# Kernel tuning notes

Measured on AMD Instinct MI355X. Metric: run time of the kernel, lower is better.

## Reference

```python
import jax, jax.numpy as jnp
import numpy as np

D = 768


def _rope(x):
    # interleaved RoPE over the FULL hidden dim (applied before head split, as in source)
    S, d = x.shape[-2], x.shape[-1]
    pos = jnp.arange(S, dtype=x.dtype)[:, None]                      # [S,1]
    theta = jnp.power(jnp.asarray(10000.0, x.dtype),
                      -2.0 * jnp.arange(d // 2, dtype=x.dtype) / d)  # [d/2]
    ang = pos * theta                                                # [S,d/2]
    cos2 = jnp.repeat(jnp.cos(ang), 2, axis=-1)                      # [S,d]
    sin2 = jnp.repeat(jnp.sin(ang), 2, axis=-1)
    x2 = jnp.stack([-x[..., 1::2], x[..., ::2]], axis=-1).reshape(x.shape)
    return x * cos2 + x2 * sin2


def _attn(q_in, kv_in, wq, bq, wk, bk, wv, bv, n_heads):
    # shared core of SelfAttention (n_heads=1) and MultiheadAttention (n_heads=8)
    B, Sq, Dm = q_in.shape
    Sk = kv_in.shape[1]
    Q = _rope(q_in @ wq + bq)
    K = _rope(kv_in @ wk + bk)
    V = kv_in @ wv + bv
    hd = Dm // n_heads
    Q = Q.reshape(B, Sq, n_heads, hd).transpose(0, 2, 1, 3)
    K = K.reshape(B, Sk, n_heads, hd).transpose(0, 2, 1, 3)
    V = V.reshape(B, Sk, n_heads, hd).transpose(0, 2, 1, 3)
    scores = jnp.einsum('bhqd,bhkd->bhqk', Q, K) * 8.0  # source multiplies by 8, no 1/sqrt(d)
    p = jax.nn.softmax(scores, axis=-1)
    out = jnp.einsum('bhqk,bhkd->bhqd', p, V)
    return out.transpose(0, 2, 1, 3).reshape(B, Sq, Dm)


def _ffn(x, w1, b1, w2, b2):
    return jax.nn.silu(x @ w1 + b1) @ w2 + b2


def _gate(x):
    # F = F * softmax(F, -1) + F
    return x * jax.nn.softmax(x, axis=-1) + x


def setup_inputs() -> dict:
    key = jax.random.key(0)
    ks = jax.random.split(key, 32)
    B, S, L = 32, 512, 100
    s = 1.0 / np.sqrt(D)

    def lin(k):
        kw, kb = jax.random.split(k)
        return (jax.random.normal(kw, (D, D), jnp.float32) * s,
                jax.random.normal(kb, (D,), jnp.float32) * 0.01)

    inp = {}
    inp['text_embedding'] = jax.random.normal(ks[0], (B, S, D), jnp.float32)
    inp['visual_ids'] = jax.random.randint(ks[1], (B, S), 0, L)
    inp['acoustic_ids'] = jax.random.randint(ks[2], (B, S), 0, L)
    # embedding tables (label_size+1 rows, last row is padding_idx -> zeros)
    vt = jax.random.normal(ks[3], (L + 1, D), jnp.float32)
    at = jax.random.normal(ks[4], (L + 1, D), jnp.float32)
    inp['vis_table'] = vt.at[L].set(0.0)
    inp['ac_table'] = at.at[L].set(0.0)
    (inp['hv_wq'], inp['hv_bq']) = lin(ks[5])
    (inp['hv_wk'], inp['hv_bk']) = lin(ks[6])
    (inp['hv_wv'], inp['hv_bv']) = lin(ks[7])
    (inp['ha_wq'], inp['ha_bq']) = lin(ks[8])
    (inp['ha_wk'], inp['ha_bk']) = lin(ks[9])
    (inp['ha_wv'], inp['ha_bv']) = lin(ks[10])
    (inp['ht_wq'], inp['ht_bq']) = lin(ks[11])
    (inp['ht_wk'], inp['ht_bk']) = lin(ks[12])
    (inp['ht_wv'], inp['ht_bv']) = lin(ks[13])
    (inp['ht_fcw'], inp['ht_fcb']) = lin(ks[14])
    (inp['ffn_w1'], inp['ffn_b1']) = lin(ks[15])
    (inp['ffn_w2'], inp['ffn_b2']) = lin(ks[16])
    kw, kb = jax.random.split(ks[17])
    inp['cat_w'] = jax.random.normal(kw, (2 * D, D), jnp.float32) * (1.0 / np.sqrt(2 * D))
    inp['cat_b'] = jax.random.normal(kb, (D,), jnp.float32) * 0.01
    return inp


def reference(text_embedding, vis_table, ac_table,
              hv_wq, hv_bq, hv_wk, hv_bk, hv_wv, hv_bv,
              ha_wq, ha_bq, ha_wk, ha_bk, ha_wv, ha_bv,
              ht_wq, ht_bq, ht_wk, ht_bk, ht_wv, ht_bv, ht_fcw, ht_fcb,
              ffn_w1, ffn_b1, ffn_w2, ffn_b2, cat_w, cat_b,
              visual_ids, acoustic_ids):
    hv = lambda q, kv: _attn(q, kv, hv_wq, hv_bq, hv_wk, hv_bk, hv_wv, hv_bv, 1)
    ha = lambda q, kv: _attn(q, kv, ha_wq, ha_bq, ha_wk, ha_bk, ha_wv, ha_bv, 1)

    visual_ = vis_table[visual_ids]       # [B,S,D]
    acoustic_ = ac_table[acoustic_ids]

    visual_ = hv(text_embedding, visual_)
    acoustic_ = ha(text_embedding, acoustic_)

    F1 = jnp.concatenate([visual_, acoustic_], axis=-1) @ cat_w + cat_b
    F1 = _ffn(_gate(F1), ffn_w1, ffn_b1, ffn_w2, ffn_b2)

    v = hv(visual_, acoustic_)
    a = ha(acoustic_, visual_)
    F2 = jnp.concatenate([v, a], axis=-1) @ cat_w + cat_b
    F2 = _ffn(_gate(F2), ffn_w1, ffn_b1, ffn_w2, ffn_b2)

    F3 = _attn(F1, text_embedding, ht_wq, ht_bq, ht_wk, ht_bk, ht_wv, ht_bv, 8)
    F3 = F3 @ ht_fcw + ht_fcb
    F3 = _ffn(_gate(F3), ffn_w1, ffn_b1, ffn_w2, ffn_b2)

    es = text_embedding + F1 + F2 + F3
    return _gate(es)
```

## Files before the change

kernel.cpp:

```cpp
#include <hip/hip_runtime.h>
#include <stdint.h>
#include <math.h>


typedef unsigned short USH;
typedef __attribute__((ext_vector_type(8))) short short8;
typedef __attribute__((ext_vector_type(4))) float floatx4;

#define MFMA16(a, b, c) __builtin_amdgcn_mfma_f32_16x16x32_bf16((a), (b), (c), 0, 0, 0)

static constexpr int NB = 32;
static constexpr int SS = 512;
static constexpr int DD = 768;
static constexpr int MM = NB * SS;

__device__ __forceinline__ float bf2f(USH h) {
    return __uint_as_float(((unsigned)h) << 16);
}
__device__ __forceinline__ USH f2bf(float x) {
    unsigned u = __float_as_uint(x);
    return (USH)((u + 0x7fffu + ((u >> 16) & 1u)) >> 16);
}
__device__ __forceinline__ void split3(float x, USH &h, USH &m, USH &l) {
    h = f2bf(x);
    const float r1 = x - bf2f(h);
    m = f2bf(r1);
    const float r2 = r1 - bf2f(m);
    l = f2bf(r2);
}
__device__ __forceinline__ void split3x8(const float* v, short8 &H, short8 &M, short8 &L) {
#pragma unroll
    for (int j = 0; j < 8; ++j) {
        USH h, m, l;
        split3(v[j], h, m, l);
        H[j] = (short)h; M[j] = (short)m; L[j] = (short)l;
    }
}
__device__ __forceinline__ uint2 pk4(USH a, USH b, USH c, USH d) {
    uint2 r;
    r.x = (unsigned)a | ((unsigned)b << 16);
    r.y = (unsigned)c | ((unsigned)d << 16);
    return r;
}

struct TransArgs {
    const float* in[13];
    USH* o0[13]; USH* o1[13]; USH* o2[13];
    int R[13];
};

__global__ __launch_bounds__(256) void trans_k(TransArgs a) {
    const int mi = blockIdx.z;
    const float* __restrict__ in = a.in[mi];
    USH* __restrict__ o0 = a.o0[mi];
    USH* __restrict__ o1 = a.o1[mi];
    USH* __restrict__ o2 = a.o2[mi];
    const int R = a.R[mi];
    const int bx = blockIdx.x, by = blockIdx.y;
    if (bx * 32 >= R) return;
    __shared__ float t[32][33];
    const int tx = threadIdx.x & 31, ty = threadIdx.x >> 5;
#pragma unroll
    for (int i = 0; i < 4; ++i)
        t[ty + i * 8][tx] = in[(size_t)(bx * 32 + ty + i * 8) * 768 + by * 32 + tx];
    __syncthreads();
#pragma unroll
    for (int i = 0; i < 4; ++i) {
        USH h, m, l;
        split3(t[tx][ty + i * 8], h, m, l);
        const size_t o = (size_t)(by * 32 + ty + i * 8) * R + bx * 32 + tx;
        o0[o] = h; o1[o] = m; o2[o] = l;
    }
}

__global__ __launch_bounds__(256) void gather_k(const int* __restrict__ ids,
                                                const float* __restrict__ table,
                                                float* __restrict__ dst) {
    const int g  = blockIdx.x * 256 + threadIdx.x;
    const int m  = g / 192;
    const int c4 = (g - m * 192) * 4;
    const int id = ids[m];
    *(float4*)(dst + (size_t)m * DD + c4) =
        *(const float4*)(table + (size_t)id * DD + c4);
}

__global__ __launch_bounds__(256) void gemm_k(
    const float* __restrict__ A0, const float* __restrict__ A1,
    const USH* __restrict__ B0, const USH* __restrict__ B1, const USH* __restrict__ B2,
    int ldb, const float* __restrict__ bias,
    float* __restrict__ C, int K, int act, int tout, int Mc)
{
    __shared__ __align__(16) USH sA0[4096], sA1[4096], sA2[4096];
    __shared__ __align__(16) USH sB0[4096], sB1[4096], sB2[4096];

    const int tid  = threadIdx.x;
    const int lane = tid & 63;
    const int w    = tid >> 6;
    const int quad = lane >> 4, l15 = lane & 15;
    const int wm = (w >> 1) * 64, wn = (w & 1) * 64;
    const int gm0 = blockIdx.x * 128, gn0 = blockIdx.y * 128;

    const int i0 = tid * 2, i1 = tid * 2 + 1;
    const int r0 = i0 >> 2, c0 = (i0 & 3) << 3;
    const int r1 = i1 >> 2, c1 = (i1 & 3) << 3;

    const floatx4 zero = {0.f, 0.f, 0.f, 0.f};
    floatx4 acc[4][4];
#pragma unroll
    for (int i = 0; i < 4; ++i)
#pragma unroll
        for (int j = 0; j < 4; ++j) acc[i][j] = zero;

    for (int k0 = 0; k0 < K; k0 += 32) {
        const float* __restrict__ A = (k0 < 768) ? A0 : A1;
        const int kof = (k0 < 768) ? k0 : (k0 - 768);

        *(uint4*)&sB0[r0 * 32 + c0] = *(const uint4*)(B0 + (size_t)(gn0 + r0) * ldb + k0 + c0);
        *(uint4*)&sB0[r1 * 32 + c1] = *(const uint4*)(B0 + (size_t)(gn0 + r1) * ldb + k0 + c1);
        *(uint4*)&sB1[r0 * 32 + c0] = *(const uint4*)(B1 + (size_t)(gn0 + r0) * ldb + k0 + c0);
        *(uint4*)&sB1[r1 * 32 + c1] = *(const uint4*)(B1 + (size_t)(gn0 + r1) * ldb + k0 + c1);
        *(uint4*)&sB2[r0 * 32 + c0] = *(const uint4*)(B2 + (size_t)(gn0 + r0) * ldb + k0 + c0);
        *(uint4*)&sB2[r1 * 32 + c1] = *(const uint4*)(B2 + (size_t)(gn0 + r1) * ldb + k0 + c1);

#pragma unroll
        for (int u = 0; u < 4; ++u) {
            const int idx = tid + u * 256;
            const int r = idx >> 3, c = (idx & 7) * 4;
            const float4 v = *(const float4*)(A + (size_t)(gm0 + r) * 768 + kof + c);
            USH h[4], m[4], l[4];
            split3(v.x, h[0], m[0], l[0]);
            split3(v.y, h[1], m[1], l[1]);
            split3(v.z, h[2], m[2], l[2]);
            split3(v.w, h[3], m[3], l[3]);
            *(uint2*)&sA0[r * 32 + c] = pk4(h[0], h[1], h[2], h[3]);
            *(uint2*)&sA1[r * 32 + c] = pk4(m[0], m[1], m[2], m[3]);
            *(uint2*)&sA2[r * 32 + c] = pk4(l[0], l[1], l[2], l[3]);
        }
        __syncthreads();

        short8 a0[4], a1f[4], a2[4], b0[4], b1f[4], b2[4];
#pragma unroll
        for (int t = 0; t < 4; ++t) {
            const int ao = (wm + t * 16 + l15) * 32 + quad * 8;
            const int bo = (wn + t * 16 + l15) * 32 + quad * 8;
            a0[t]  = *(const short8*)&sA0[ao];
            a1f[t] = *(const short8*)&sA1[ao];
            a2[t]  = *(const short8*)&sA2[ao];
            b0[t]  = *(const short8*)&sB0[bo];
            b1f[t] = *(const short8*)&sB1[bo];
            b2[t]  = *(const short8*)&sB2[bo];
        }
#pragma unroll
        for (int i = 0; i < 4; ++i)
#pragma unroll
            for (int j = 0; j < 4; ++j) acc[i][j] = MFMA16(a0[i],  b0[j],  acc[i][j]);
#pragma unroll
        for (int i = 0; i < 4; ++i)
#pragma unroll
            for (int j = 0; j < 4; ++j) acc[i][j] = MFMA16(a0[i],  b1f[j], acc[i][j]);
#pragma unroll
        for (int i = 0; i < 4; ++i)
#pragma unroll
            for (int j = 0; j < 4; ++j) acc[i][j] = MFMA16(a1f[i], b0[j],  acc[i][j]);
#pragma unroll
        for (int i = 0; i < 4; ++i)
#pragma unroll
            for (int j = 0; j < 4; ++j) acc[i][j] = MFMA16(a0[i],  b2[j],  acc[i][j]);
#pragma unroll
        for (int i = 0; i < 4; ++i)
#pragma unroll
            for (int j = 0; j < 4; ++j) acc[i][j] = MFMA16(a2[i],  b0[j],  acc[i][j]);
#pragma unroll
        for (int i = 0; i < 4; ++i)
#pragma unroll
            for (int j = 0; j < 4; ++j) acc[i][j] = MFMA16(a1f[i], b1f[j], acc[i][j]);
        __syncthreads();
    }

#pragma unroll
    for (int j = 0; j < 4; ++j) {
        const int col = gn0 + wn + j * 16 + l15;
        const float bv = bias[col];
#pragma unroll
        for (int i = 0; i < 4; ++i) {
#pragma unroll
            for (int r = 0; r < 4; ++r) {
                const int row = gm0 + wm + i * 16 + quad * 4 + r;
                float x = acc[i][j][r] + bv;
                if (act == 1) {
                    const float s = 1.0f / (1.0f + expf(-x));
                    x = x * s;
                }
                const size_t o = tout ? ((size_t)col * Mc + row)
                                      : ((size_t)row * 768 + col);
                C[o] = x;
            }
        }
    }
}

__global__ __launch_bounds__(256) void rope_k(float* __restrict__ X) {
    const int p = blockIdx.x * 256 + threadIdx.x;
    const int m = p / 384;
    const int i = p - m * 384;
    const int s = m & (SS - 1);
    const float ef = (-2.0f * (float)i) / 768.0f;
    const float th = (float)pow(10000.0, (double)ef);
    const float ang = (float)s * th;
    float sn, cs;
    sincosf(ang, &sn, &cs);
    float2 x = *(float2*)(X + (size_t)m * DD + 2 * i);
    float2 y;
    y.x = x.x * cs - x.y * sn;
    y.y = x.y * cs + x.x * sn;
    *(float2*)(X + (size_t)m * DD + 2 * i) = y;
}

__global__ __launch_bounds__(256) void attn_k(
    const float* __restrict__ Q, const float* __restrict__ Kp,
    const float* __restrict__ Vt, float* __restrict__ O,
    int H, int hd, int Mc)
{
    __shared__ __align__(16) float S[16][520];
    __shared__ __align__(16) USH P2buf[16 * 520];
    __shared__ float red[16][16];
    __shared__ float stat[16];

    const int tid  = threadIdx.x;
    const int lane = tid & 63;
    const int w    = tid >> 6;
    const int quad = lane >> 4, l15 = lane & 15;
    const int b = blockIdx.y / H;
    const int h = blockIdx.y - b * H;
    const int q0 = blockIdx.x * 16;

    const floatx4 zero = {0.f, 0.f, 0.f, 0.f};

    floatx4 acc[8];
#pragma unroll
    for (int t = 0; t < 8; ++t) acc[t] = zero;

    const size_t qbase = ((size_t)(b * SS + q0 + l15)) * DD + h * hd;
    const int nks = hd >> 5;
    for (int ks = 0; ks < nks; ++ks) {
        const int co = ks * 32 + quad * 8;
        float qv[8];
        *(float4*)&qv[0] = *(const float4*)(Q + qbase + co);
        *(float4*)&qv[4] = *(const float4*)(Q + qbase + co + 4);
        short8 qh, qm, ql;
        split3x8(qv, qh, qm, ql);
#pragma unroll
        for (int t = 0; t < 8; ++t) {
            const size_t kb = ((size_t)(b * SS + w * 128 + t * 16 + l15)) * DD + h * hd + co;
            float kv[8];
            *(float4*)&kv[0] = *(const float4*)(Kp + kb);
            *(float4*)&kv[4] = *(const float4*)(Kp + kb + 4);
            short8 kh, km, kl;
            split3x8(kv, kh, km, kl);
            acc[t] = MFMA16(qh, kh, acc[t]);
            acc[t] = MFMA16(qh, km, acc[t]);
            acc[t] = MFMA16(qm, kh, acc[t]);
            acc[t] = MFMA16(qh, kl, acc[t]);
            acc[t] = MFMA16(ql, kh, acc[t]);
            acc[t] = MFMA16(qm, km, acc[t]);
        }
    }
#pragma unroll
    for (int t = 0; t < 8; ++t)
#pragma unroll
        for (int r = 0; r < 4; ++r)
            S[quad * 4 + r][w * 128 + t * 16 + l15] = acc[t][r] * 8.0f;
    __syncthreads();

    const int row = tid >> 4, c16 = tid & 15;
    const int cb = c16 * 32;
    float mx = -3.4e38f;
#pragma unroll 8
    for (int c = 0; c < 32; ++c) mx = fmaxf(mx, S[row][cb + c]);
    red[row][c16] = mx;
    __syncthreads();
    if (c16 == 0) {
        float m2 = red[row][0];
#pragma unroll
        for (int j = 1; j < 16; ++j) m2 = fmaxf(m2, red[row][j]);
        stat[row] = m2;
    }
    __syncthreads();
    mx = stat[row];
    float ev[32];
    float sum = 0.f;
#pragma unroll 8
    for (int c = 0; c < 32; ++c) {
        ev[c] = expf(S[row][cb + c] - mx);
        sum += ev[c];
    }
    red[row][c16] = sum;
    __syncthreads();
    if (c16 == 0) {
        float s2 = 0.f;
#pragma unroll
        for (int j = 0; j < 16; ++j) s2 += red[row][j];
        stat[row] = s2;
    }
    __syncthreads();
    const float den = stat[row];
    USH* const P0 = (USH*)&S[0][0];
    USH* const P1 = P0 + 16 * 520;
    USH* const P2 = P2buf;
#pragma unroll 8
    for (int c = 0; c < 32; ++c) {
        const float pr = ev[c] / den;
        USH hh, mm, ll;
        split3(pr, hh, mm, ll);
        P0[row * 520 + cb + c] = hh;
        P1[row * 520 + cb + c] = mm;
        P2[row * 520 + cb + c] = ll;
    }
    __syncthreads();

    const int nnt = hd >> 4;
    for (int nt = w; nt < nnt; nt += 4) {
        floatx4 o = zero;
        const int colg = h * hd + nt * 16 + l15;
        const size_t vb = (size_t)colg * Mc + b * SS;
        for (int ks = 0; ks < 16; ++ks) {
            const int ko = ks * 32 + quad * 8;
            const short8 ph = *(const short8*)&P0[l15 * 520 + ko];
            const short8 pm = *(const short8*)&P1[l15 * 520 + ko];
            const short8 pl = *(const short8*)&P2[l15 * 520 + ko];
            float vv[8];
            *(float4*)&vv[0] = *(const float4*)(Vt + vb + ko);
            *(float4*)&vv[4] = *(const float4*)(Vt + vb + ko + 4);
            short8 vh, vm, vl;
            split3x8(vv, vh, vm, vl);
            o = MFMA16(ph, vh, o);
            o = MFMA16(ph, vm, o);
            o = MFMA16(pm, vh, o);
            o = MFMA16(ph, vl, o);
            o = MFMA16(pl, vh, o);
            o = MFMA16(pm, vm, o);
        }
#pragma unroll
        for (int r = 0; r < 4; ++r) {
            const int orow = b * SS + q0 + quad * 4 + r;
            O[(size_t)orow * 768 + colg] = o[r];
        }
    }
}

__global__ __launch_bounds__(256) void gate_k(float* __restrict__ X) {
    __shared__ float red[256];
    const int r = blockIdx.x, tid = threadIdx.x;
    const size_t base = (size_t)r * DD;
    float x[3];
#pragma unroll
    for (int j = 0; j < 3; ++j) x[j] = X[base + tid + j * 256];
    float mx = fmaxf(x[0], fmaxf(x[1], x[2]));
    red[tid] = mx;
    __syncthreads();
    for (int s = 128; s > 0; s >>= 1) {
        if (tid < s) red[tid] = fmaxf(red[tid], red[tid + s]);
        __syncthreads();
    }
    mx = red[0];
    __syncthreads();
    float e[3];
    float sum = 0.f;
#pragma unroll
    for (int j = 0; j < 3; ++j) { e[j] = expf(x[j] - mx); sum += e[j]; }
    red[tid] = sum;
    __syncthreads();
    for (int s = 128; s > 0; s >>= 1) {
        if (tid < s) red[tid] += red[tid + s];
        __syncthreads();
    }
    const float den = red[0];
#pragma unroll
    for (int j = 0; j < 3; ++j)
        X[base + tid + j * 256] = x[j] * (e[j] / den) + x[j];
}

__global__ __launch_bounds__(256) void final_k(
    const float* __restrict__ text,
    const float* __restrict__ F1, const float* __restrict__ F2,
    const float* __restrict__ F3, float* __restrict__ out)
{
    __shared__ float red[256];
    const int r = blockIdx.x, tid = threadIdx.x;
    const size_t base = (size_t)r * DD;
    float x[3];
#pragma unroll
    for (int j = 0; j < 3; ++j) {
        const int c = tid + j * 256;
        x[j] = ((text[base + c] + F1[base + c]) + F2[base + c]) + F3[base + c];
    }
    float mx = fmaxf(x[0], fmaxf(x[1], x[2]));
    red[tid] = mx;
    __syncthreads();
    for (int s = 128; s > 0; s >>= 1) {
        if (tid < s) red[tid] = fmaxf(red[tid], red[tid + s]);
        __syncthreads();
    }
    mx = red[0];
    __syncthreads();
    float e[3];
    float sum = 0.f;
#pragma unroll
    for (int j = 0; j < 3; ++j) { e[j] = expf(x[j] - mx); sum += e[j]; }
    red[tid] = sum;
    __syncthreads();
    for (int s = 128; s > 0; s >>= 1) {
        if (tid < s) red[tid] += red[tid + s];
        __syncthreads();
    }
    const float den = red[0];
#pragma unroll
    for (int j = 0; j < 3; ++j) {
        const int c = tid + j * 256;
        out[base + c] = x[j] * (e[j] / den) + x[j];
    }
}

extern "C" void kernel_launch(void* const* d_in, const int* in_sizes, int n_in,
                              void* d_out, int out_size, void* d_ws, size_t ws_size,
                              hipStream_t stream)
{
    (void)in_sizes; (void)n_in; (void)out_size;

    const float* text    = (const float*)d_in[0];
    const int*   vis_ids = (const int*)d_in[1];
    const int*   ac_ids  = (const int*)d_in[2];
    const float* vis_tab = (const float*)d_in[3];
    const float* ac_tab  = (const float*)d_in[4];
    const float* hv_wq = (const float*)d_in[5],  *hv_bq = (const float*)d_in[6];
    const float* hv_wk = (const float*)d_in[7],  *hv_bk = (const float*)d_in[8];
    const float* hv_wv = (const float*)d_in[9],  *hv_bv = (const float*)d_in[10];
    const float* ha_wq = (const float*)d_in[11], *ha_bq = (const float*)d_in[12];
    const float* ha_wk = (const float*)d_in[13], *ha_bk = (const float*)d_in[14];
    const float* ha_wv = (const float*)d_in[15], *ha_bv = (const float*)d_in[16];
    const float* ht_wq = (const float*)d_in[17], *ht_bq = (const float*)d_in[18];
    const float* ht_wk = (const float*)d_in[19], *ht_bk = (const float*)d_in[20];
    const float* ht_wv = (const float*)d_in[21], *ht_bv = (const float*)d_in[22];
    const float* ht_fcw = (const float*)d_in[23], *ht_fcb = (const float*)d_in[24];
    const float* ffn_w1 = (const float*)d_in[25], *ffn_b1 = (const float*)d_in[26];
    const float* ffn_w2 = (const float*)d_in[27], *ffn_b2 = (const float*)d_in[28];
    const float* cat_w  = (const float*)d_in[29], *cat_b  = (const float*)d_in[30];

    const size_t SQ   = (size_t)768 * 768;
    const size_t WUSH = 3 * (12 * SQ + (size_t)768 * 1536);
    int Mc = 0;
    for (int cand = MM; cand >= 512; cand >>= 1) {
        const size_t need = WUSH * sizeof(USH) + (size_t)6 * cand * 768 * sizeof(float);
        if (need <= ws_size) { Mc = cand; break; }
    }
    if (Mc == 0) return;
    const int nchunk = MM / Mc;
    const int chB    = Mc / SS;

    USH* p = (USH*)d_ws;
    USH *wt0[13], *wt1[13], *wt2[13];
    for (int i = 0; i < 13; ++i) {
        const size_t sz = (i == 12) ? (size_t)768 * 1536 : SQ;
        wt0[i] = p; p += sz;
        wt1[i] = p; p += sz;
        wt2[i] = p; p += sz;
    }
    const size_t PSZ = (size_t)Mc * 768;
    float* fp = (float*)p;
    float *A_ = fp + 0 * PSZ, *B_ = fp + 1 * PSZ, *C_ = fp + 2 * PSZ;
    float *D_ = fp + 3 * PSZ, *E_ = fp + 4 * PSZ, *F_ = fp + 5 * PSZ;

    TransArgs ta;
    const float* tin[13] = {hv_wq, hv_wk, hv_wv, ha_wq, ha_wk, ha_wv,
                            ht_wq, ht_wk, ht_wv, ht_fcw, ffn_w1, ffn_w2, cat_w};
    for (int i = 0; i < 13; ++i) {
        ta.in[i] = tin[i]; ta.o0[i] = wt0[i]; ta.o1[i] = wt1[i]; ta.o2[i] = wt2[i];
        ta.R[i] = (i == 12) ? 1536 : 768;
    }
    trans_k<<<dim3(48, 24, 13), 256, 0, stream>>>(ta);

    const dim3 gg(Mc / 128, DD / 128), gb(256);
    const int ropeg = Mc * 384 / 256;
    const float* NULF = nullptr;

#define GEMM(A0P, A1P, WI, LDB, BIAS, CP, KK, ACT, TOUT) \
    gemm_k<<<gg, gb, 0, stream>>>(A0P, A1P, wt0[WI], wt1[WI], wt2[WI], LDB, BIAS, CP, KK, ACT, TOUT, Mc)
#define ROPE(XP) rope_k<<<ropeg, 256, 0, stream>>>(XP)
#define ATTN(QP, KP, VP, OP, HH, HD) \
    attn_k<<<dim3(SS / 16, chB * (HH)), 256, 0, stream>>>(QP, KP, VP, OP, HH, HD, Mc)
#define GATE(XP) gate_k<<<Mc, 256, 0, stream>>>(XP)

    for (int c = 0; c < nchunk; ++c) {
        const float* tx = text + (size_t)c * PSZ;
        const int* vi = vis_ids + (size_t)c * Mc;
        const int* ai = ac_ids  + (size_t)c * Mc;
        float* outc = (float*)d_out + (size_t)c * PSZ;

        gather_k<<<Mc * 192 / 256, 256, 0, stream>>>(vi, vis_tab, A_);
        gather_k<<<Mc * 192 / 256, 256, 0, stream>>>(ai, ac_tab, B_);

        GEMM(tx, NULF, 0, 768, hv_bq, C_, 768, 0, 0);
        GEMM(A_, NULF, 1, 768, hv_bk, D_, 768, 0, 0);
        GEMM(A_, NULF, 2, 768, hv_bv, E_, 768, 0, 1);
        ROPE(C_); ROPE(D_);
        ATTN(C_, D_, E_, F_, 1, 768);

        GEMM(tx, NULF, 3, 768, ha_bq, C_, 768, 0, 0);
        GEMM(B_, NULF, 4, 768, ha_bk, D_, 768, 0, 0);
        GEMM(B_, NULF, 5, 768, ha_bv, E_, 768, 0, 1);
        ROPE(C_); ROPE(D_);
        ATTN(C_, D_, E_, A_, 1, 768);

        GEMM(F_, NULF, 0, 768, hv_bq, C_, 768, 0, 0);
        GEMM(A_, NULF, 1, 768, hv_bk, D_, 768, 0, 0);
        GEMM(A_, NULF, 2, 768, hv_bv, E_, 768, 0, 1);
        ROPE(C_); ROPE(D_);
        ATTN(C_, D_, E_, C_, 1, 768);

        GEMM(A_, NULF, 3, 768, ha_bq, B_, 768, 0, 0);
        GEMM(F_, NULF, 4, 768, ha_bk, D_, 768, 0, 0);
        GEMM(F_, NULF, 5, 768, ha_bv, E_, 768, 0, 1);
        ROPE(B_); ROPE(D_);
        ATTN(B_, D_, E_, B_, 1, 768);

        GEMM(F_, A_, 12, 1536, cat_b, D_, 1536, 0, 0);
        GATE(D_);
        GEMM(D_, NULF, 10, 768, ffn_b1, E_, 768, 1, 0);
        GEMM(E_, NULF, 11, 768, ffn_b2, F_, 768, 0, 0);

        GEMM(C_, B_, 12, 1536, cat_b, A_, 1536, 0, 0);
        GATE(A_);
        GEMM(A_, NULF, 10, 768, ffn_b1, C_, 768, 1, 0);
        GEMM(C_, NULF, 11, 768, ffn_b2, B_, 768, 0, 0);

        GEMM(F_, NULF, 6, 768, ht_bq, C_, 768, 0, 0);
        GEMM(tx, NULF, 7, 768, ht_bk, D_, 768, 0, 0);
        GEMM(tx, NULF, 8, 768, ht_bv, E_, 768, 0, 1);
        ROPE(C_); ROPE(D_);
        ATTN(C_, D_, E_, C_, 8, 96);
        GEMM(C_, NULF, 9, 768, ht_fcb, A_, 768, 0, 0);
        GATE(A_);
        GEMM(A_, NULF, 10, 768, ffn_b1, C_, 768, 1, 0);
        GEMM(C_, NULF, 11, 768, ffn_b2, D_, 768, 0, 0);

        final_k<<<Mc, 256, 0, stream>>>(tx, F_, B_, D_, outc);
    }

#undef GEMM
#undef ROPE
#undef ATTN
#undef GATE
}
```

Measured before the change: 6.833 ms.

## Pre-split K/V into bf16 triples and use precomputed RoPE table in attention

Adds a fast path in which the V projection GEMM writes its transposed output directly as three bf16 split planes, and the K RoPE kernel likewise emits bf16 split planes. A new attention kernel then loads these pre-split operands instead of splitting K and V inside every attention block. RoPE cos/sin values are precomputed once into a table, which replaces the per-element pow/sincos. The output buffer serves as scratch, and the path needs more workspace, otherwise it falls back to the old path.

```diff
diff --git a/kernel.cpp b/kernel.cpp
--- a/kernel.cpp
+++ b/kernel.cpp
@@ -88,7 +88,8 @@
     const float* __restrict__ A0, const float* __restrict__ A1,
     const USH* __restrict__ B0, const USH* __restrict__ B1, const USH* __restrict__ B2,
     int ldb, const float* __restrict__ bias,
-    float* __restrict__ C, int K, int act, int tout, int Mc)
+    float* __restrict__ C, USH* __restrict__ S0p, USH* __restrict__ S1p,
+    USH* __restrict__ S2p, int K, int act, int tout, int Mc)
 {
     __shared__ __align__(16) USH sA0[4096], sA1[4096], sA2[4096];
     __shared__ __align__(16) USH sB0[4096], sB1[4096], sB2[4096];
@@ -191,12 +192,32 @@
                     const float s = 1.0f / (1.0f + expf(-x));
                     x = x * s;
                 }
-                const size_t o = tout ? ((size_t)col * Mc + row)
-                                      : ((size_t)row * 768 + col);
-                C[o] = x;
+                if (tout == 1) {
+                    USH hh, mm2, ll;
+                    split3(x, hh, mm2, ll);
+                    const size_t o = (size_t)col * Mc + row;
+                    S0p[o] = hh; S1p[o] = mm2; S2p[o] = ll;
+                } else if (tout == 2) {
+                    C[(size_t)col * Mc + row] = x;
+                } else {
+                    C[(size_t)row * 768 + col] = x;
+                }
             }
         }
     }
+}
+
+__global__ __launch_bounds__(256) void tab_k(float* __restrict__ tab) {
+    const int p = blockIdx.x * 256 + threadIdx.x;
+    const int s = p / 384;
+    const int i = p - s * 384;
+    const float ef = (-2.0f * (float)i) / 768.0f;
+    const float th = (float)pow(10000.0, (double)ef);
+    const float ang = (float)s * th;
+    float sn, cs;
+    sincosf(ang, &sn, &cs);
+    tab[2 * p]     = cs;
+    tab[2 * p + 1] = sn;
 }
 
 __global__ __launch_bounds__(256) void rope_k(float* __restrict__ X) {
@@ -214,6 +235,183 @@
     y.x = x.x * cs - x.y * sn;
     y.y = x.y * cs + x.x * sn;
     *(float2*)(X + (size_t)m * DD + 2 * i) = y;
+}
+
+__global__ __launch_bounds__(256) void rope_tab_k(float* __restrict__ X,
+                                                  const float* __restrict__ tab) {
+    const int p = blockIdx.x * 256 + threadIdx.x;
+    const int m = p / 384;
+    const int i = p - m * 384;
+    const int s = m & (SS - 1);
+    const float2 t = *(const float2*)(tab + 2 * (s * 384 + i));
+    float2 x = *(float2*)(X + (size_t)m * DD + 2 * i);
+    float2 y;
+    y.x = x.x * t.x - x.y * t.y;
+    y.y = x.y * t.x + x.x * t.y;
+    *(float2*)(X + (size_t)m * DD + 2 * i) = y;
+}
+
+__global__ __launch_bounds__(256) void rope_split_tab_k(
+    const float* __restrict__ X, const float* __restrict__ tab,
+    USH* __restrict__ P0, USH* __restrict__ P1, USH* __restrict__ P2)
+{
+    const int p = blockIdx.x * 256 + threadIdx.x;
+    const int m = p / 384;
+    const int i = p - m * 384;
+    const int s = m & (SS - 1);
+    const float2 t = *(const float2*)(tab + 2 * (s * 384 + i));
+    const float2 x = *(const float2*)(X + (size_t)m * DD + 2 * i);
+    float2 y;
+    y.x = x.x * t.x - x.y * t.y;
+    y.y = x.y * t.x + x.x * t.y;
+    USH h0, m0, l0, h1, m1, l1;
+    split3(y.x, h0, m0, l0);
+    split3(y.y, h1, m1, l1);
+    const size_t o = (size_t)m * DD + 2 * i;
+    *(unsigned*)&P0[o] = (unsigned)h0 | ((unsigned)h1 << 16);
+    *(unsigned*)&P1[o] = (unsigned)m0 | ((unsigned)m1 << 16);
+    *(unsigned*)&P2[o] = (unsigned)l0 | ((unsigned)l1 << 16);
+}
+
+__global__ __launch_bounds__(256) void attn_fast_k(
+    const float* __restrict__ Q,
+    const USH* __restrict__ KH, const USH* __restrict__ KM, const USH* __restrict__ KL,
+    const USH* __restrict__ VH, const USH* __restrict__ VM, const USH* __restrict__ VL,
+    float* __restrict__ O, int H, int hd, int Mc)
+{
+    __shared__ __align__(16) float S[16][520];
+    __shared__ __align__(16) USH P2buf[16 * 520];
+    __shared__ float red[16][16];
+    __shared__ float stat[16];
+
+    const int tid  = threadIdx.x;
+    const int lane = tid & 63;
+    const int w    = tid >> 6;
+    const int quad = lane >> 4, l15 = lane & 15;
+    const int b = blockIdx.y / H;
+    const int h = blockIdx.y - b * H;
+    const int q0 = blockIdx.x * 16;
+
+    const floatx4 zero = {0.f, 0.f, 0.f, 0.f};
+
+    floatx4 acc[8];
+#pragma unroll
+    for (int t = 0; t < 8; ++t) acc[t] = zero;
+
+    const size_t qbase  = ((size_t)(b * SS + q0 + l15)) * DD + h * hd;
+    const size_t kstrip = ((size_t)(b * SS + w * 128 + l15)) * DD + h * hd;
+    const int nks = hd >> 5;
+    for (int ks = 0; ks < nks; ++ks) {
+        const int co = ks * 32 + quad * 8;
+        float qv[8];
+        *(float4*)&qv[0] = *(const float4*)(Q + qbase + co);
+        *(float4*)&qv[4] = *(const float4*)(Q + qbase + co + 4);
+        short8 qh, qm, ql;
+        split3x8(qv, qh, qm, ql);
+
+        size_t ka = kstrip + co;
+        short8 khc = *(const short8*)&KH[ka];
+        short8 kmc = *(const short8*)&KM[ka];
+        short8 klc = *(const short8*)&KL[ka];
+#pragma unroll
+        for (int t = 0; t < 8; ++t) {
+            short8 khn = khc, kmn = kmc, kln = klc;
+            if (t < 7) {
+                const size_t kb = ka + (size_t)(t + 1) * 16 * DD;
+                khn = *(const short8*)&KH[kb];
+                kmn = *(const short8*)&KM[kb];
+                kln = *(const short8*)&KL[kb];
+            }
+            acc[t] = MFMA16(qh, khc, acc[t]);
+            acc[t] = MFMA16(qh, kmc, acc[t]);
+            acc[t] = MFMA16(qm, khc, acc[t]);
+            acc[t] = MFMA16(qh, klc, acc[t]);
+            acc[t] = MFMA16(ql, khc, acc[t]);
+            acc[t] = MFMA16(qm, kmc, acc[t]);
+            __builtin_amdgcn_sched_barrier(0);
+            khc = khn; kmc = kmn; klc = kln;
+        }
+    }
+#pragma unroll
+    for (int t = 0; t < 8; ++t)
+#pragma unroll
+        for (int r = 0; r < 4; ++r)
+            S[quad * 4 + r][w * 128 + t * 16 + l15] = acc[t][r] * 8.0f;
+    __syncthreads();
+
+    const int row = tid >> 4, c16 = tid & 15;
+    const int cb = c16 * 32;
+    float mx = -3.4e38f;
+#pragma unroll 8
+    for (int c = 0; c < 32; ++c) mx = fmaxf(mx, S[row][cb + c]);
+    red[row][c16] = mx;
+    __syncthreads();
+    if (c16 == 0) {
+        float m2 = red[row][0];
+#pragma unroll
+        for (int j = 1; j < 16; ++j) m2 = fmaxf(m2, red[row][j]);
+        stat[row] = m2;
+    }
+    __syncthreads();
+    mx = stat[row];
+    float ev[32];
+    float sum = 0.f;
+#pragma unroll 8
+    for (int c = 0; c < 32; ++c) {
+        ev[c] = expf(S[row][cb + c] - mx);
+        sum += ev[c];
+    }
+    red[row][c16] = sum;
+    __syncthreads();
+    if (c16 == 0) {
+        float s2 = 0.f;
+#pragma unroll
+        for (int j = 0; j < 16; ++j) s2 += red[row][j];
+        stat[row] = s2;
+    }
+    __syncthreads();
+    const float den = stat[row];
+    USH* const P0 = (USH*)&S[0][0];
+    USH* const P1 = P0 + 16 * 520;
+    USH* const P2 = P2buf;
+#pragma unroll 8
+    for (int c = 0; c < 32; ++c) {
+        const float pr = ev[c] / den;
+        USH hh, mm, ll;
+        split3(pr, hh, mm, ll);
+        P0[row * 520 + cb + c] = hh;
+        P1[row * 520 + cb + c] = mm;
+        P2[row * 520 + cb + c] = ll;
+    }
+    __syncthreads();
+
+    const int nnt = hd >> 4;
+    for (int nt = w; nt < nnt; nt += 4) {
+        floatx4 o = zero;
+        const int colg = h * hd + nt * 16 + l15;
+        const size_t vb = (size_t)colg * Mc + b * SS;
+#pragma unroll 2
+        for (int ks = 0; ks < 16; ++ks) {
+            const int ko = ks * 32 + quad * 8;
+            const short8 ph = *(const short8*)&P0[l15 * 520 + ko];
+            const short8 pm = *(const short8*)&P1[l15 * 520 + ko];
+            const short8 pl = *(const short8*)&P2[l15 * 520 + ko];
+            const short8 vh = *(const short8*)&VH[vb + ko];
+            const short8 vm = *(const short8*)&VM[vb + ko];
+            const short8 vl = *(const short8*)&VL[vb + ko];
+            o = MFMA16(ph, vh, o);
+            o = MFMA16(ph, vm, o);
+            o = MFMA16(pm, vh, o);
+            o = MFMA16(ph, vl, o);
+            o = MFMA16(pl, vh, o);
+            o = MFMA16(pm, vm, o);
+        }
+#pragma unroll
+        for (int r = 0; r < 4; ++r) {
+            const int orow = b * SS + q0 + quad * 4 + r;
+            O[(size_t)orow * 768 + colg] = o[r];
+        }
+    }
 }
 
 __global__ __launch_bounds__(256) void attn_k(
@@ -448,10 +646,13 @@
 
     const size_t SQ   = (size_t)768 * 768;
     const size_t WUSH = 3 * (12 * SQ + (size_t)768 * 1536);
-    int Mc = 0;
+    const size_t TABF = (size_t)512 * 384 * 2;
+    int Mc = 0, fast = 0;
     for (int cand = MM; cand >= 512; cand >>= 1) {
-        const size_t need = WUSH * sizeof(USH) + (size_t)6 * cand * 768 * sizeof(float);
-        if (need <= ws_size) { Mc = cand; break; }
+        const size_t nf = WUSH * sizeof(USH) + TABF * 4 + (size_t)cand * 768 * 28;
+        const size_t ns = WUSH * sizeof(USH) + (size_t)cand * 768 * 24;
+        if (nf <= ws_size) { Mc = cand; fast = 1; break; }
+        if (ns <= ws_size) { Mc = cand; fast = 0; break; }
     }
     if (Mc == 0) return;
     const int nchunk = MM / Mc;
@@ -465,10 +666,6 @@
         wt1[i] = p; p += sz;
         wt2[i] = p; p += sz;
     }
-    const size_t PSZ = (size_t)Mc * 768;
-    float* fp = (float*)p;
-    float *A_ = fp + 0 * PSZ, *B_ = fp + 1 * PSZ, *C_ = fp + 2 * PSZ;
-    float *D_ = fp + 3 * PSZ, *E_ = fp + 4 * PSZ, *F_ = fp + 5 * PSZ;
 
     TransArgs ta;
     const float* tin[13] = {hv_wq, hv_wk, hv_wv, ha_wq, ha_wk, ha_wv,
@@ -479,75 +676,168 @@
     }
     trans_k<<<dim3(48, 24, 13), 256, 0, stream>>>(ta);
 
+    const size_t PSZ = (size_t)Mc * 768;
     const dim3 gg(Mc / 128, DD / 128), gb(256);
     const int ropeg = Mc * 384 / 256;
     const float* NULF = nullptr;
+    USH* const NUSH = nullptr;
+
+    if (fast) {
+        float* tab = (float*)p;
+        float* fp  = tab + TABF;
+        float *A_ = fp + 0 * PSZ, *B_ = fp + 1 * PSZ;
+        float *C_ = fp + 2 * PSZ, *F_ = fp + 3 * PSZ;
+        USH* KH = (USH*)(fp + 4 * PSZ);
+        USH* KM = KH + PSZ;  USH* KL = KM + PSZ;
+        USH* VH = KL + PSZ;  USH* VM = VH + PSZ;  USH* VL = VM + PSZ;
+
+        tab_k<<<(512 * 384) / 256, 256, 0, stream>>>(tab);
+
+#define GEMM(A0P, A1P, WI, LDB, BIAS, CP, KK, ACT) \
+    gemm_k<<<gg, gb, 0, stream>>>(A0P, A1P, wt0[WI], wt1[WI], wt2[WI], LDB, BIAS, \
+                                  CP, NUSH, NUSH, NUSH, KK, ACT, 0, Mc)
+#define GEMMV(A0P, WI, BIAS) \
+    gemm_k<<<gg, gb, 0, stream>>>(A0P, NULF, wt0[WI], wt1[WI], wt2[WI], 768, BIAS, \
+                                  (float*)nullptr, VH, VM, VL, 768, 0, 1, Mc)
+#define ROPE(XP)  rope_tab_k<<<ropeg, 256, 0, stream>>>(XP, tab)
+#define RSPL(XP)  rope_split_tab_k<<<ropeg, 256, 0, stream>>>(XP, tab, KH, KM, KL)
+#define ATTNF(QP, OP, HH, HD) \
+    attn_fast_k<<<dim3(SS / 16, chB * (HH)), 256, 0, stream>>>(QP, KH, KM, KL, \
+                                                  VH, VM, VL, OP, HH, HD, Mc)
+#define GATE(XP) gate_k<<<Mc, 256, 0, stream>>>(XP)
+
+        for (int c = 0; c < nchunk; ++c) {
+            const float* tx = text + (size_t)c * PSZ;
+            const int* vi = vis_ids + (size_t)c * Mc;
+            const int* ai = ac_ids  + (size_t)c * Mc;
+            float* outc = (float*)d_out + (size_t)c * PSZ;
+
+            gather_k<<<Mc * 192 / 256, 256, 0, stream>>>(vi, vis_tab, A_);
+            gather_k<<<Mc * 192 / 256, 256, 0, stream>>>(ai, ac_tab, B_);
+
+            GEMM(tx, NULF, 0, 768, hv_bq, C_, 768, 0);
+            GEMM(A_, NULF, 1, 768, hv_bk, outc, 768, 0);
+            GEMMV(A_, 2, hv_bv);
+            ROPE(C_); RSPL(outc);
+            ATTNF(C_, F_, 1, 768);
+
+            GEMM(tx, NULF, 3, 768, ha_bq, C_, 768, 0);
+            GEMM(B_, NULF, 4, 768, ha_bk, outc, 768, 0);
+            GEMMV(B_, 5, ha_bv);
+            ROPE(C_); RSPL(outc);
+            ATTNF(C_, A_, 1, 768);
+
+            GEMM(F_, NULF, 0, 768, hv_bq, C_, 768, 0);
+            GEMM(A_, NULF, 1, 768, hv_bk, outc, 768, 0);
+            GEMMV(A_, 2, hv_bv);
+            ROPE(C_); RSPL(outc);
+            ATTNF(C_, C_, 1, 768);
+
+            GEMM(A_, NULF, 3, 768, ha_bq, B_, 768, 0);
+            GEMM(F_, NULF, 4, 768, ha_bk, outc, 768, 0);
+            GEMMV(F_, 5, ha_bv);
+            ROPE(B_); RSPL(outc);
+            ATTNF(B_, B_, 1, 768);
+
+            GEMM(F_, A_, 12, 1536, cat_b, outc, 1536, 0);
+            GATE(outc);
+            GEMM(outc, NULF, 10, 768, ffn_b1, F_, 768, 1);
+            GEMM(F_, NULF, 11, 768, ffn_b2, A_, 768, 0);
+
+            GEMM(C_, B_, 12, 1536, cat_b, outc, 1536, 0);
+            GATE(outc);
+            GEMM(outc, NULF, 10, 768, ffn_b1, F_, 768, 1);
+            GEMM(F_, NULF, 11, 768, ffn_b2, C_, 768, 0);
+
+            GEMM(A_, NULF, 6, 768, ht_bq, B_, 768, 0);
+            GEMM(tx, NULF, 7, 768, ht_bk, outc, 768, 0);
+            GEMMV(tx, 8, ht_bv);
+            ROPE(B_); RSPL(outc);
+            ATTNF(B_, B_, 8, 96);
+            GEMM(B_, NULF, 9, 768, ht_fcb, F_, 768, 0);
+            GATE(F_);
+            GEMM(F_, NULF, 10, 768, ffn_b1, B_, 768, 1);
+            GEMM(B_, NULF, 11, 768, ffn_b2, F_, 768, 0);
+
+            final_k<<<Mc, 256, 0, stream>>>(tx, A_, C_, F_, outc);
+        }
+#undef GEMM
+#undef GEMMV
+#undef ROPE
+#undef RSPL
+#undef ATTNF
+#undef GATE
+    } else {
+        float* fp = (float*)p;
+        float *A_ = fp + 0 * PSZ, *B_ = fp + 1 * PSZ, *C_ = fp + 2 * PSZ;
+        float *D_ = fp + 3 * PSZ, *E_ = fp + 4 * PSZ, *F_ = fp + 5 * PSZ;
 
 #define GEMM(A0P, A1P, WI, LDB, BIAS, CP, KK, ACT, TOUT) \
-    gemm_k<<<gg, gb, 0, stream>>>(A0P, A1P, wt0[WI], wt1[WI], wt2[WI], LDB, BIAS, CP, KK, ACT, TOUT, Mc)
+    gemm_k<<<gg, gb, 0, stream>>>(A0P, A1P, wt0[WI], wt1[WI], wt2[WI], LDB, BIAS, \
+                                  CP, NUSH, NUSH, NUSH, KK, ACT, TOUT, Mc)
 #define ROPE(XP) rope_k<<<ropeg, 256, 0, stream>>>(XP)
 #define ATTN(QP, KP, VP, OP, HH, HD) \
     attn_k<<<dim3(SS / 16, chB * (HH)), 256, 0, stream>>>(QP, KP, VP, OP, HH, HD, Mc)
 #define GATE(XP) gate_k<<<Mc, 256, 0, stream>>>(XP)
 
-    for (int c = 0; c < nchunk; ++c) {
-        const float* tx = text + (size_t)c * PSZ;
-        const int* vi = vis_ids + (size_t)c * Mc;
-        const int* ai = ac_ids  + (size_t)c * Mc;
-        float* outc = (float*)d_out + (size_t)c * PSZ;
-
-        gather_k<<<Mc * 192 / 256, 256, 0, stream>>>(vi, vis_tab, A_);
-        gather_k<<<Mc * 192 / 256, 256, 0, stream>>>(ai, ac_tab, B_);
-
-        GEMM(tx, NULF, 0, 768, hv_bq, C_, 768, 0, 0);
-        GEMM(A_, NULF, 1, 768, hv_bk, D_, 768, 0, 0);
-        GEMM(A_, NULF, 2, 768, hv_bv, E_, 768, 0, 1);
-        ROPE(C_); ROPE(D_);
-        ATTN(C_, D_, E_, F_, 1, 768);
-
-        GEMM(tx, NULF, 3, 768, ha_bq, C_, 768, 0, 0);
-        GEMM(B_, NULF, 4, 768, ha_bk, D_, 768, 0, 0);
-        GEMM(B_, NULF, 5, 768, ha_bv, E_, 768, 0, 1);
-        ROPE(C_); ROPE(D_);
-        ATTN(C_, D_, E_, A_, 1, 768);
-
-        GEMM(F_, NULF, 0, 768, hv_bq, C_, 768, 0, 0);
-        GEMM(A_, NULF, 1, 768, hv_bk, D_, 768, 0, 0);
-        GEMM(A_, NULF, 2, 768, hv_bv, E_, 768, 0, 1);
-        ROPE(C_); ROPE(D_);
-        ATTN(C_, D_, E_, C_, 1, 768);
-
-        GEMM(A_, NULF, 3, 768, ha_bq, B_, 768, 0, 0);
-        GEMM(F_, NULF, 4, 768, ha_bk, D_, 768, 0, 0);
-        GEMM(F_, NULF, 5, 768, ha_bv, E_, 768, 0, 1);
-        ROPE(B_); ROPE(D_);
-        ATTN(B_, D_, E_, B_, 1, 768);
-
-        GEMM(F_, A_, 12, 1536, cat_b, D_, 1536, 0, 0);
-        GATE(D_);
-        GEMM(D_, NULF, 10, 768, ffn_b1, E_, 768, 1, 0);
-        GEMM(E_, NULF, 11, 768, ffn_b2, F_, 768, 0, 0);
-
-        GEMM(C_, B_, 12, 1536, cat_b, A_, 1536, 0, 0);
-        GATE(A_);
-        GEMM(A_, NULF, 10, 768, ffn_b1, C_, 768, 1, 0);
-        GEMM(C_, NULF, 11, 768, ffn_b2, B_, 768, 0, 0);
-
-        GEMM(F_, NULF, 6, 768, ht_bq, C_, 768, 0, 0);
-        GEMM(tx, NULF, 7, 768, ht_bk, D_, 768, 0, 0);
-        GEMM(tx, NULF, 8, 768, ht_bv, E_, 768, 0, 1);
-        ROPE(C_); ROPE(D_);
-        ATTN(C_, D_, E_, C_, 8, 96);
-        GEMM(C_, NULF, 9, 768, ht_fcb, A_, 768, 0, 0);
-        GATE(A_);
-        GEMM(A_, NULF, 10, 768, ffn_b1, C_, 768, 1, 0);
-        GEMM(C_, NULF, 11, 768, ffn_b2, D_, 768, 0, 0);
-
-        final_k<<<Mc, 256, 0, stream>>>(tx, F_, B_, D_, outc);
-    }
-
+        for (int c = 0; c < nchunk; ++c) {
+            const float* tx = text + (size_t)c * PSZ;
+            const int* vi = vis_ids + (size_t)c * Mc;
+            const int* ai = ac_ids  + (size_t)c * Mc;
+            float* outc = (float*)d_out + (size_t)c * PSZ;
+
+            gather_k<<<Mc * 192 / 256, 256, 0, stream>>>(vi, vis_tab, A_);
+            gather_k<<<Mc * 192 / 256, 256, 0, stream>>>(ai, ac_tab, B_);
+
+            GEMM(tx, NULF, 0, 768, hv_bq, C_, 768, 0, 0);
+            GEMM(A_, NULF, 1, 768, hv_bk, D_, 768, 0, 0);
+            GEMM(A_, NULF, 2, 768, hv_bv, E_, 768, 0, 2);
+            ROPE(C_); ROPE(D_);
+            ATTN(C_, D_, E_, F_, 1, 768);
+
+            GEMM(tx, NULF, 3, 768, ha_bq, C_, 768, 0, 0);
+            GEMM(B_, NULF, 4, 768, ha_bk, D_, 768, 0, 0);
+            GEMM(B_, NULF, 5, 768, ha_bv, E_, 768, 0, 2);
+            ROPE(C_); ROPE(D_);
+            ATTN(C_, D_, E_, A_, 1, 768);
+
+            GEMM(F_, NULF, 0, 768, hv_bq, C_, 768, 0, 0);
+            GEMM(A_, NULF, 1, 768, hv_bk, D_, 768, 0, 0);
+            GEMM(A_, NULF, 2, 768, hv_bv, E_, 768, 0, 2);
+            ROPE(C_); ROPE(D_);
+            ATTN(C_, D_, E_, C_, 1, 768);
+
+            GEMM(A_, NULF, 3, 768, ha_bq, B_, 768, 0, 0);
+            GEMM(F_, NULF, 4, 768, ha_bk, D_, 768, 0, 0);
+            GEMM(F_, NULF, 5, 768, ha_bv, E_, 768, 0, 2);
+            ROPE(B_); ROPE(D_);
+            ATTN(B_, D_, E_, B_, 1, 768);
+
+            GEMM(F_, A_, 12, 1536, cat_b, D_, 1536, 0, 0);
+            GATE(D_);
+            GEMM(D_, NULF, 10, 768, ffn_b1, E_, 768, 1, 0);
+            GEMM(E_, NULF, 11, 768, ffn_b2, F_, 768, 0, 0);
+
+            GEMM(C_, B_, 12, 1536, cat_b, A_, 1536, 0, 0);
+            GATE(A_);
+            GEMM(A_, NULF, 10, 768, ffn_b1, C_, 768, 1, 0);
+            GEMM(C_, NULF, 11, 768, ffn_b2, B_, 768, 0, 0);
+
+            GEMM(F_, NULF, 6, 768, ht_bq, C_, 768, 0, 0);
+            GEMM(tx, NULF, 7, 768, ht_bk, D_, 768, 0, 0);
+            GEMM(tx, NULF, 8, 768, ht_bv, E_, 768, 0, 2);
+            ROPE(C_); ROPE(D_);
+            ATTN(C_, D_, E_, C_, 8, 96);
+            GEMM(C_, NULF, 9, 768, ht_fcb, A_, 768, 0, 0);
+            GATE(A_);
+            GEMM(A_, NULF, 10, 768, ffn_b1, C_, 768, 1, 0);
+            GEMM(C_, NULF, 11, 768, ffn_b2, D_, 768, 0, 0);
+
+            final_k<<<Mc, 256, 0, stream>>>(tx, F_, B_, D_, outc);
+        }
 #undef GEMM
 #undef ROPE
 #undef ATTN
 #undef GATE
-}
+    }
+}
```

Result: slower. 7.340 ms (+7.4%).
